# Kernel tuning notes

Measured on AMD Instinct MI355X. Metric: run time of the kernel, lower is better.

Reference implementation:

```python
import jax, jax.numpy as jnp
import numpy as np

BS, NS, D, H = 4, 1024, 2048, 16
DH = D // H
SCALE = DH ** -0.5
MASK_BIAS = -1e9


def setup_inputs() -> dict:
    key = jax.random.key(0)
    k1, k2, k3, k4, k5 = jax.random.split(key, 5)
    x = jax.random.normal(k1, (BS, NS, D), dtype=jnp.float32)
    attention_ids = jax.random.randint(k2, (BS, NS), 0, 2, dtype=jnp.int32)
    # torch.nn.Linear weights: [out_features, in_features]
    w_in = jax.random.normal(k3, (3 * D, D), dtype=jnp.float32) * (D ** -0.5)
    w_out = jax.random.normal(k4, (D, D), dtype=jnp.float32) * (D ** -0.5)
    b_out = jax.random.normal(k5, (D,), dtype=jnp.float32) * 0.02
    return {"x": x, "attention_ids": attention_ids, "w_in": w_in,
            "w_out": w_out, "b_out": b_out}


def reference(x, attention_ids, w_in, w_out, b_out):
    bs, ns, _ = x.shape
    qkv = jnp.einsum('bsd,ed->bse', x, w_in)            # [bs, ns, 3*D]
    qkv = qkv.reshape(bs, ns, 3, H, DH).transpose(2, 0, 3, 1, 4)
    q, k, v = qkv[0], qkv[1], qkv[2]                     # [bs, H, ns, DH]
    attn = jnp.einsum('bhqd,bhkd->bhqk', q, k)           # [bs, H, ns, ns]
    # NOTE: mask bias added BEFORE the scale multiply, as in the source.
    bias = (attention_ids.astype(attn.dtype) * MASK_BIAS)[:, None, None, :]
    attn = jax.nn.softmax((attn + bias) * SCALE, axis=-1)
    out = jnp.einsum('bhqk,bhkd->bhqd', attn, v)         # [bs, H, ns, DH]
    out = out.transpose(0, 2, 1, 3).reshape(bs, ns, D)
    return jnp.einsum('bsd,ed->bse', out, w_out) + b_out
```

## Files before the change

kernel.cpp:

```cpp
#include <hip/hip_runtime.h>
#include <hip/hip_bf16.h>
#include <stdint.h>

typedef __bf16 bf16;
typedef __bf16 bf16x8 __attribute__((ext_vector_type(8)));
typedef __bf16 bf16x4 __attribute__((ext_vector_type(4)));
typedef float floatx4 __attribute__((ext_vector_type(4)));

#define NSEQ   1024
#define DM     2048
#define NH     16
#define DHD    128
#define E3     6144
#define SCALE_F 0.08838834764831845f
#define MBIAS_S (-1.0e9f * SCALE_F)
#define NEG_HUGE (-3.0e38f)

static __device__ __forceinline__ floatx4 mfma16(bf16x8 a, bf16x8 b, floatx4 c) {
  return __builtin_amdgcn_mfma_f32_16x16x32_bf16(a, b, c, 0, 0, 0);
}

static __device__ __forceinline__ void load_lds16(const bf16* g, bf16* l) {
  __builtin_amdgcn_global_load_lds(
      (__attribute__((address_space(1))) const void*)g,
      (__attribute__((address_space(3))) void*)l, 16, 0, 0);
}

__global__ __launch_bounds__(256) void cast_bf16_kernel(const float* __restrict__ in,
                                                        bf16* __restrict__ out) {
  int i = blockIdx.x * 256 + threadIdx.x;
  float4 v = ((const float4*)in)[i];
  bf16x4 o;
  o[0] = (bf16)v.x; o[1] = (bf16)v.y; o[2] = (bf16)v.z; o[3] = (bf16)v.w;
  ((bf16x4*)out)[i] = o;
}

template <typename OutT>
__global__ __launch_bounds__(256) void gemm_bt_kernel(
    const bf16* __restrict__ A, const bf16* __restrict__ B,
    OutT* __restrict__ C, const float* __restrict__ bias,
    int N, int K) {
  __shared__ bf16 As[128 * 32];
  __shared__ bf16 Bs[128 * 32];
  const int ntn = N >> 7;
  const int tm = blockIdx.x / ntn;
  const int tn = blockIdx.x - tm * ntn;
  const int tid = threadIdx.x;
  const int w = tid >> 6;
  const int lane = tid & 63;
  const int lq = lane & 15;
  const int lg = lane >> 4;
  const int wr = w >> 1;
  const int wc = w & 1;

  const bf16* Ag = A + (size_t)(tm * 128) * K;
  const bf16* Bg = B + (size_t)(tn * 128) * K;
  const int c0 = tid, c1 = tid + 256;
  const int r0 = c0 >> 2, o0 = (c0 & 3) * 8;
  const int r1 = c1 >> 2, o1 = (c1 & 3) * 8;
  bf16* lA0 = As + w * 512;
  bf16* lA1 = As + w * 512 + 2048;
  bf16* lB0 = Bs + w * 512;
  bf16* lB1 = Bs + w * 512 + 2048;

  floatx4 acc[4][4] = {};

  for (int k0 = 0; k0 < K; k0 += 32) {
    load_lds16(Ag + (size_t)r0 * K + k0 + o0, lA0);
    load_lds16(Ag + (size_t)r1 * K + k0 + o1, lA1);
    load_lds16(Bg + (size_t)r0 * K + k0 + o0, lB0);
    load_lds16(Bg + (size_t)r1 * K + k0 + o1, lB1);
    __syncthreads();
    bf16x8 af[4], bfr[4];
#pragma unroll
    for (int m = 0; m < 4; m++)
      af[m] = *(const bf16x8*)(As + (wr * 64 + m * 16 + lq) * 32 + lg * 8);
#pragma unroll
    for (int n = 0; n < 4; n++)
      bfr[n] = *(const bf16x8*)(Bs + (wc * 64 + n * 16 + lq) * 32 + lg * 8);
#pragma unroll
    for (int m = 0; m < 4; m++)
#pragma unroll
      for (int n = 0; n < 4; n++)
        acc[m][n] = mfma16(af[m], bfr[n], acc[m][n]);
    __syncthreads();
  }

#pragma unroll
  for (int n = 0; n < 4; n++) {
    const int ccol = tn * 128 + wc * 64 + n * 16 + lq;
    const float bv = bias ? bias[ccol] : 0.f;
#pragma unroll
    for (int m = 0; m < 4; m++) {
      const size_t rbase = (size_t)(tm * 128 + wr * 64 + m * 16 + lg * 4);
#pragma unroll
      for (int r = 0; r < 4; r++)
        C[(rbase + r) * N + ccol] = (OutT)(acc[m][n][r] + bv);
    }
  }
}

__global__ __launch_bounds__(256) void vtrans_kernel(const bf16* __restrict__ qkv,
                                                     bf16* __restrict__ vt) {
  const int bid = blockIdx.x;
  const int sblk = bid & 7;
  const int h = (bid >> 3) & 15;
  const int b = bid >> 7;
  const int t = threadIdx.x;
  const int dhb = (t & 7) | (((t >> 6) & 1) << 3);
  const int sb  = ((t >> 3) & 7) | (((t >> 7) & 1) << 3);
  const int s0 = sblk * 128 + sb * 8;
  const int dh0 = dhb * 8;
  const bf16* src = qkv + (size_t)(b * NSEQ + s0) * E3 + 2 * DM + h * DHD + dh0;
  bf16x8 r[8];
#pragma unroll
  for (int i = 0; i < 8; i++) r[i] = *(const bf16x8*)(src + (size_t)i * E3);
  bf16* dst = vt + ((size_t)(b * NH + h) * DHD + dh0) * NSEQ + s0;
#pragma unroll
  for (int j = 0; j < 8; j++) {
    bf16x8 o;
#pragma unroll
    for (int i = 0; i < 8; i++) o[i] = r[i][j];
    *(bf16x8*)(dst + (size_t)j * NSEQ) = o;
  }
}

__global__ __launch_bounds__(256) void attn_kernel(
    const bf16* __restrict__ qkv, const bf16* __restrict__ vt,
    const int* __restrict__ ids, bf16* __restrict__ ao) {
  __shared__ bf16 Ksh[2][64 * 128];
  __shared__ bf16 Vsh[2][128 * 64];
  __shared__ bf16 plds[4][16][72];
  const int bid = blockIdx.x;
  const int qt = bid & 15;
  const int h = (bid >> 4) & 15;
  const int b = bid >> 8;
  const int tid = threadIdx.x;
  const int w = tid >> 6;
  const int lane = tid & 63;
  const int lq = lane & 15;
  const int lg = lane >> 4;
  const int q0 = qt * 64 + w * 16;
  const int swz = (lq & 7) << 4;

  const int krow0 = w * 16 + (lane >> 4);
  const int kc = lane & 15;
  const int vrow0 = w * 32 + (lane >> 3);
  const int vc = lane & 7;
  const int vr7 = (lane >> 3) & 7;

  const bf16* kg = qkv + DM + h * DHD;
  const bf16* vg = vt + (size_t)(b * NH + h) * DHD * NSEQ;

  auto stage = [&](int buf, int k0) {
#pragma unroll
    for (int i = 0; i < 4; i++) {
      const int kr = krow0 + i * 4;
      load_lds16(kg + (size_t)(b * NSEQ + k0 + kr) * E3 + ((kc ^ (kr & 7)) * 8),
                 &Ksh[buf][(w * 16 + i * 4) * 128]);
    }
#pragma unroll
    for (int i = 0; i < 4; i++) {
      const int vr = vrow0 + i * 8;
      load_lds16(vg + (size_t)vr * NSEQ + k0 + ((vc ^ vr7) * 8),
                 &Vsh[buf][(w * 32 + i * 8) * 64]);
    }
  };

  bf16x8 qf[4];
  const bf16* qb = qkv + (size_t)(b * NSEQ + q0 + lq) * E3 + h * DHD + lg * 8;
#pragma unroll
  for (int kk = 0; kk < 4; kk++) qf[kk] = *(const bf16x8*)(qb + kk * 32);

  floatx4 acc[8] = {};
  float M[4], L[4];
#pragma unroll
  for (int r = 0; r < 4; r++) { M[r] = NEG_HUGE; L[r] = 0.f; }

  bf16 (*pw)[72] = plds[w];
  const int* idb = ids + b * NSEQ;

  stage(0, 0);
  __syncthreads();
  int cur = 0;

  for (int t = 0; t < 16; t++) {
    const int k0 = t * 64;
    if (t < 15) stage(cur ^ 1, k0 + 64);

    const bf16* Kc = Ksh[cur];
    floatx4 s[4] = {};
#pragma unroll
    for (int n = 0; n < 4; n++) {
      const int krow = n * 16 + lq;
#pragma unroll
      for (int kk = 0; kk < 4; kk++) {
        bf16x8 kf = *(const bf16x8*)(Kc + krow * 128 +
                                     (((kk * 64 + lg * 16) ^ swz) >> 1));
        s[n] = mfma16(qf[kk], kf, s[n]);
      }
    }
    float sa[4][4], pm[4];
#pragma unroll
    for (int r = 0; r < 4; r++) pm[r] = NEG_HUGE;
#pragma unroll
    for (int n = 0; n < 4; n++) {
      const float bv = idb[k0 + n * 16 + lq] ? MBIAS_S : 0.f;
#pragma unroll
      for (int r = 0; r < 4; r++) {
        sa[n][r] = s[n][r] * SCALE_F + bv;
        pm[r] = fmaxf(pm[r], sa[n][r]);
      }
    }
#pragma unroll
    for (int m = 1; m <= 8; m <<= 1)
#pragma unroll
      for (int r = 0; r < 4; r++) pm[r] = fmaxf(pm[r], __shfl_xor(pm[r], m, 64));
    float corr[4];
#pragma unroll
    for (int r = 0; r < 4; r++) {
      const float mn = fmaxf(M[r], pm[r]);
      corr[r] = __expf(M[r] - mn);
      M[r] = mn;
    }
    float rs[4] = {0.f, 0.f, 0.f, 0.f};
#pragma unroll
    for (int n = 0; n < 4; n++)
#pragma unroll
      for (int r = 0; r < 4; r++) {
        const float p = __expf(sa[n][r] - M[r]);
        sa[n][r] = p;
        rs[r] += p;
      }
#pragma unroll
    for (int m = 1; m <= 8; m <<= 1)
#pragma unroll
      for (int r = 0; r < 4; r++) rs[r] += __shfl_xor(rs[r], m, 64);
#pragma unroll
    for (int r = 0; r < 4; r++) L[r] = L[r] * corr[r] + rs[r];
#pragma unroll
    for (int n8 = 0; n8 < 8; n8++)
#pragma unroll
      for (int r = 0; r < 4; r++) acc[n8][r] *= corr[r];
#pragma unroll
    for (int n = 0; n < 4; n++)
#pragma unroll
      for (int r = 0; r < 4; r++) pw[lg * 4 + r][n * 16 + lq] = (bf16)sa[n][r];
    bf16x8 pf0 = *(const bf16x8*)(&pw[lq][lg * 8]);
    bf16x8 pf1 = *(const bf16x8*)(&pw[lq][32 + lg * 8]);
    const bf16* Vc = Vsh[cur];
#pragma unroll
    for (int n8 = 0; n8 < 8; n8++) {
      const int vrow = n8 * 16 + lq;
      bf16x8 v0 = *(const bf16x8*)(Vc + vrow * 64 + (((lg * 16) ^ swz) >> 1));
      bf16x8 v1 = *(const bf16x8*)(Vc + vrow * 64 + (((64 + lg * 16) ^ swz) >> 1));
      acc[n8] = mfma16(pf0, v0, acc[n8]);
      acc[n8] = mfma16(pf1, v1, acc[n8]);
    }
    __syncthreads();
    cur ^= 1;
  }

  float inv[4];
#pragma unroll
  for (int r = 0; r < 4; r++) inv[r] = 1.f / L[r];
  bf16* aob = ao + (size_t)(b * NSEQ + q0 + lg * 4) * DM + h * DHD + lq;
#pragma unroll
  for (int n8 = 0; n8 < 8; n8++)
#pragma unroll
    for (int r = 0; r < 4; r++)
      aob[(size_t)r * DM + n8 * 16] = (bf16)(acc[n8][r] * inv[r]);
}

extern "C" void kernel_launch(void* const* d_in, const int* in_sizes, int n_in,
                              void* d_out, int out_size, void* d_ws, size_t ws_size,
                              hipStream_t stream) {
  const float* x     = (const float*)d_in[0];
  const int*   ids   = (const int*)d_in[1];
  const float* w_in  = (const float*)d_in[2];
  const float* w_out = (const float*)d_in[3];
  const float* b_out = (const float*)d_in[4];
  float* out = (float*)d_out;

  bf16* ws  = (bf16*)d_ws;
  bf16* xb  = ws;
  bf16* wib = xb  + (size_t)4096 * 2048;
  bf16* wob = wib + (size_t)6144 * 2048;
  bf16* qkv = wob + (size_t)2048 * 2048;
  bf16* vtb = qkv + (size_t)4096 * 6144;
  bf16* aob = vtb + (size_t)4 * 16 * 128 * 1024;

  cast_bf16_kernel<<<8192, 256, 0, stream>>>(x, xb);
  cast_bf16_kernel<<<12288, 256, 0, stream>>>(w_in, wib);
  cast_bf16_kernel<<<4096, 256, 0, stream>>>(w_out, wob);
  gemm_bt_kernel<bf16><<<32 * 48, 256, 0, stream>>>(xb, wib, qkv, nullptr, 6144, 2048);
  vtrans_kernel<<<512, 256, 0, stream>>>(qkv, vtb);
  attn_kernel<<<1024, 256, 0, stream>>>(qkv, vtb, ids, aob);
  gemm_bt_kernel<float><<<32 * 16, 256, 0, stream>>>(aob, wob, out, b_out, 2048, 2048);
}
```

Baseline: 323.3 us.

## Fuse cast kernels, defer softmax rescale, and raise MFMA wave priority

Merges the three fp32-to-bf16 cast launches into a single kernel that picks its source by block index, removing two launches. In the attention loop, the running-max update and the accumulator rescale are skipped unless some row's new max exceeds the stored one by more than a threshold, applied wave-wide. This saves exps and multiplies on most tiles. The QK and PV MFMA sections are wrapped in s_setprio to favour matrix issue. Deferred rescaling lets exp arguments reach up to about e^8 before renormalisation, which fp32 accumulators can hold but which slightly changes the bf16 rounding of P.

```diff
diff --git a/kernel.cpp b/kernel.cpp
--- a/kernel.cpp
+++ b/kernel.cpp
@@ -15,6 +15,7 @@
 #define SCALE_F 0.08838834764831845f
 #define MBIAS_S (-1.0e9f * SCALE_F)
 #define NEG_HUGE (-3.0e38f)
+#define DEFER_THR 8.0f
 
 static __device__ __forceinline__ floatx4 mfma16(bf16x8 a, bf16x8 b, floatx4 c) {
   return __builtin_amdgcn_mfma_f32_16x16x32_bf16(a, b, c, 0, 0, 0);
@@ -26,13 +27,22 @@
       (__attribute__((address_space(3))) void*)l, 16, 0, 0);
 }
 
-__global__ __launch_bounds__(256) void cast_bf16_kernel(const float* __restrict__ in,
-                                                        bf16* __restrict__ out) {
-  int i = blockIdx.x * 256 + threadIdx.x;
-  float4 v = ((const float4*)in)[i];
+__global__ __launch_bounds__(256) void cast3_kernel(
+    const float* __restrict__ x, const float* __restrict__ wi,
+    const float* __restrict__ wo, bf16* __restrict__ xb,
+    bf16* __restrict__ wib, bf16* __restrict__ wob) {
+  const int blk = blockIdx.x;
+  const float* src;
+  bf16* dst;
+  int base;
+  if (blk < 8192)       { src = x;  dst = xb;  base = blk; }
+  else if (blk < 20480) { src = wi; dst = wib; base = blk - 8192; }
+  else                  { src = wo; dst = wob; base = blk - 20480; }
+  const int i = base * 256 + threadIdx.x;
+  float4 v = ((const float4*)src)[i];
   bf16x4 o;
   o[0] = (bf16)v.x; o[1] = (bf16)v.y; o[2] = (bf16)v.z; o[3] = (bf16)v.w;
-  ((bf16x4*)out)[i] = o;
+  ((bf16x4*)dst)[i] = o;
 }
 
 template <typename OutT>
@@ -190,6 +200,7 @@
 
     const bf16* Kc = Ksh[cur];
     floatx4 s[4] = {};
+    __builtin_amdgcn_s_setprio(1);
 #pragma unroll
     for (int n = 0; n < 4; n++) {
       const int krow = n * 16 + lq;
@@ -200,6 +211,7 @@
         s[n] = mfma16(qf[kk], kf, s[n]);
       }
     }
+    __builtin_amdgcn_s_setprio(0);
     float sa[4][4], pm[4];
 #pragma unroll
     for (int r = 0; r < 4; r++) pm[r] = NEG_HUGE;
@@ -216,12 +228,19 @@
     for (int m = 1; m <= 8; m <<= 1)
 #pragma unroll
       for (int r = 0; r < 4; r++) pm[r] = fmaxf(pm[r], __shfl_xor(pm[r], m, 64));
+
+    int grew = 0;
+#pragma unroll
+    for (int r = 0; r < 4; r++) grew |= (pm[r] > M[r] + DEFER_THR) ? 1 : 0;
+    const bool full = __any(grew);
     float corr[4];
-#pragma unroll
-    for (int r = 0; r < 4; r++) {
-      const float mn = fmaxf(M[r], pm[r]);
-      corr[r] = __expf(M[r] - mn);
-      M[r] = mn;
+    if (full) {
+#pragma unroll
+      for (int r = 0; r < 4; r++) {
+        const float mn = fmaxf(M[r], pm[r]);
+        corr[r] = __expf(M[r] - mn);
+        M[r] = mn;
+      }
     }
     float rs[4] = {0.f, 0.f, 0.f, 0.f};
 #pragma unroll
@@ -236,12 +255,17 @@
     for (int m = 1; m <= 8; m <<= 1)
 #pragma unroll
       for (int r = 0; r < 4; r++) rs[r] += __shfl_xor(rs[r], m, 64);
-#pragma unroll
-    for (int r = 0; r < 4; r++) L[r] = L[r] * corr[r] + rs[r];
-#pragma unroll
-    for (int n8 = 0; n8 < 8; n8++)
-#pragma unroll
-      for (int r = 0; r < 4; r++) acc[n8][r] *= corr[r];
+    if (full) {
+#pragma unroll
+      for (int r = 0; r < 4; r++) L[r] = L[r] * corr[r] + rs[r];
+#pragma unroll
+      for (int n8 = 0; n8 < 8; n8++)
+#pragma unroll
+        for (int r = 0; r < 4; r++) acc[n8][r] *= corr[r];
+    } else {
+#pragma unroll
+      for (int r = 0; r < 4; r++) L[r] += rs[r];
+    }
 #pragma unroll
     for (int n = 0; n < 4; n++)
 #pragma unroll
@@ -249,6 +273,7 @@
     bf16x8 pf0 = *(const bf16x8*)(&pw[lq][lg * 8]);
     bf16x8 pf1 = *(const bf16x8*)(&pw[lq][32 + lg * 8]);
     const bf16* Vc = Vsh[cur];
+    __builtin_amdgcn_s_setprio(1);
 #pragma unroll
     for (int n8 = 0; n8 < 8; n8++) {
       const int vrow = n8 * 16 + lq;
@@ -257,6 +282,7 @@
       acc[n8] = mfma16(pf0, v0, acc[n8]);
       acc[n8] = mfma16(pf1, v1, acc[n8]);
     }
+    __builtin_amdgcn_s_setprio(0);
     __syncthreads();
     cur ^= 1;
   }
@@ -290,9 +316,7 @@
   bf16* vtb = qkv + (size_t)4096 * 6144;
   bf16* aob = vtb + (size_t)4 * 16 * 128 * 1024;
 
-  cast_bf16_kernel<<<8192, 256, 0, stream>>>(x, xb);
-  cast_bf16_kernel<<<12288, 256, 0, stream>>>(w_in, wib);
-  cast_bf16_kernel<<<4096, 256, 0, stream>>>(w_out, wob);
+  cast3_kernel<<<24576, 256, 0, stream>>>(x, w_in, w_out, xb, wib, wob);
   gemm_bt_kernel<bf16><<<32 * 48, 256, 0, stream>>>(xb, wib, qkv, nullptr, 6144, 2048);
   vtrans_kernel<<<512, 256, 0, stream>>>(qkv, vtb);
   attn_kernel<<<1024, 256, 0, stream>>>(qkv, vtb, ids, aob);
```

After: 321.4 us. No clear change (-0.6%).
